# Optimization experiments

Hardware: AMD Instinct MI355X
Metric: run time of the kernel (lower is better)

The kernel has to match this reference:

```python
import jax, jax.numpy as jnp
import numpy as np

B, S, D = 2, 2048, 2048
H, KV, HD = 16, 8, 128
G = H // KV          # GQA group size
EPS = 1e-6
SCALE = HD ** -0.5


def setup_inputs() -> dict:
    key = jax.random.key(0)
    ks = jax.random.split(key, 8)
    x = jax.random.normal(ks[0], (B, S, D), dtype=jnp.float32)
    # RoPE tables (theta = 1e6, Qwen3-style), shape [B, S, HD]
    inv_freq = 1.0 / (1e6 ** (np.arange(0, HD, 2, dtype=np.float32) / HD))
    ang = np.arange(S, dtype=np.float32)[:, None] * inv_freq[None, :]   # [S, HD/2]
    emb = np.concatenate([ang, ang], axis=-1)                            # [S, HD]
    cos = jnp.broadcast_to(jnp.asarray(np.cos(emb)), (B, S, HD))
    sin = jnp.broadcast_to(jnp.asarray(np.sin(emb)), (B, S, HD))
    # additive causal mask [B, 1, S, S]
    causal = jnp.where(jnp.tril(jnp.ones((S, S), dtype=bool)), 0.0, -1e9).astype(jnp.float32)
    attention_mask = jnp.broadcast_to(causal[None, None], (B, 1, S, S))
    std = D ** -0.5
    wq = jax.random.normal(ks[1], (H * HD, D), dtype=jnp.float32) * std
    wk = jax.random.normal(ks[2], (KV * HD, D), dtype=jnp.float32) * std
    wv = jax.random.normal(ks[3], (KV * HD, D), dtype=jnp.float32) * std
    wo = jax.random.normal(ks[4], (D, H * HD), dtype=jnp.float32) * (H * HD) ** -0.5
    q_norm_w = jnp.ones((HD,), dtype=jnp.float32)
    k_norm_w = jnp.ones((HD,), dtype=jnp.float32)
    return {"x": x, "cos": cos, "sin": sin, "attention_mask": attention_mask,
            "wq": wq, "wk": wk, "wv": wv, "wo": wo,
            "q_norm_w": q_norm_w, "k_norm_w": k_norm_w}


def _rmsnorm(x, w):
    xf = x.astype(jnp.float32)
    var = jnp.mean(xf * xf, axis=-1, keepdims=True)
    return w * (xf * jax.lax.rsqrt(var + EPS)).astype(x.dtype)


def _rotate_half(x):
    x1, x2 = jnp.split(x, 2, axis=-1)
    return jnp.concatenate([-x2, x1], axis=-1)


def _rope(q, k, cos, sin):
    # q: [B,H,S,HD], k: [B,KV,S,HD]; cos/sin: [B,S,HD] -> [B,1,S,HD]
    c, s = cos[:, None], sin[:, None]
    return q * c + _rotate_half(q) * s, k * c + _rotate_half(k) * s


def reference(x, cos, sin, attention_mask, wq, wk, wv, wo, q_norm_w, k_norm_w):
    # projections -> [B, heads, S, HD]
    q = (x @ wq.T).reshape(B, S, H, HD).transpose(0, 2, 1, 3)
    k = (x @ wk.T).reshape(B, S, KV, HD).transpose(0, 2, 1, 3)
    v = (x @ wv.T).reshape(B, S, KV, HD).transpose(0, 2, 1, 3)
    q = _rmsnorm(q, q_norm_w)
    k = _rmsnorm(k, k_norm_w)
    q, k = _rope(q, k, cos, sin)
    # GQA: view q as [B, KV, G, S, HD]; contract against shared KV heads
    q5 = q.reshape(B, KV, G, S, HD)
    scores = jnp.einsum('bkgqd,bktd->bkgqt', q5, k) * SCALE       # [B,KV,G,S,S]
    scores = scores + attention_mask[:, :, None]                   # [B,1,1,S,S] broadcast
    attn = jax.nn.softmax(scores.astype(jnp.float32), axis=-1).astype(q.dtype)
    out = jnp.einsum('bkgqt,bktd->bkgqd', attn, v)                 # [B,KV,G,S,HD]
    out = out.reshape(B, H, S, HD).transpose(0, 2, 1, 3).reshape(B, S, H * HD)
    attn_output = out @ wo.T
    return attn_output, attn.reshape(B, H, S, S)
```

## Files before the change

kernel.cpp:

```cpp
#include <hip/hip_runtime.h>

#define B_  2
#define S_  2048
#define D_  2048
#define H_  16
#define KV_ 8
#define HD_ 128
#define SCALE_ 0.08838834764831845f

typedef __attribute__((ext_vector_type(8))) short sh8;
typedef __attribute__((ext_vector_type(4))) float f32x4;
typedef unsigned short u16;
typedef unsigned int u32;

__device__ __forceinline__ u16 f2bf(float f){
  u32 u = __float_as_uint(f);
  u += 0x7fffu + ((u >> 16) & 1u);
  return (u16)(u >> 16);
}
__device__ __forceinline__ float bf2f(u16 h){
  return __uint_as_float(((u32)h) << 16);
}
__device__ __forceinline__ void gl_lds16(const u16* g, u16* l){
  __builtin_amdgcn_global_load_lds(
      (const __attribute__((address_space(1))) u32*)g,
      (__attribute__((address_space(3))) u32*)l, 16, 0, 0);
}

__global__ void cvt_bf16(const float* __restrict__ in, u16* __restrict__ out, int n){
  int i = (blockIdx.x * blockDim.x + threadIdx.x) * 4;
  const int stride = gridDim.x * blockDim.x * 4;
  for (; i < n; i += stride){
    float4 f = *(const float4*)(in + i);
    ushort4 u;
    u.x = f2bf(f.x); u.y = f2bf(f.y); u.z = f2bf(f.z); u.w = f2bf(f.w);
    *(ushort4*)(out + i) = u;
  }
}

template<int MODE>
__global__ __launch_bounds__(256, 2) void gemm_bt(
    const u16* __restrict__ A, const u16* __restrict__ Bq,
    const u16* __restrict__ Bk, const u16* __restrict__ Bv,
    u16* __restrict__ Oq, u16* __restrict__ Ok, u16* __restrict__ Ov,
    float* __restrict__ Of, int K)
{
  __shared__ __align__(16) u16 As[128*32];
  __shared__ __align__(16) u16 Bs[128*32];
  const int m0 = blockIdx.y * 128, n0 = blockIdx.x * 128;
  const u16* Bp; int nb;
  if (MODE == 0){
    if      (n0 < 2048){ Bp = Bq; nb = n0;        }
    else if (n0 < 3072){ Bp = Bk; nb = n0 - 2048; }
    else               { Bp = Bv; nb = n0 - 3072; }
  } else { Bp = Bq; nb = n0; }
  const int tid = threadIdx.x, lane = tid & 63, w = tid >> 6;
  const int wr = w >> 1, wc = w & 1, lg = lane >> 4, l15 = lane & 15;
  const int srow = lane >> 2, skof = (lane & 3) * 8;
  f32x4 acc[4][4];
  #pragma unroll
  for (int i = 0; i < 4; ++i)
    #pragma unroll
    for (int j = 0; j < 4; ++j) acc[i][j] = (f32x4){0.f,0.f,0.f,0.f};
  const int nkt = K >> 5;
  for (int kt = 0; kt < nkt; ++kt){
    const int k0 = kt << 5;
    __syncthreads();
    #pragma unroll
    for (int c = 0; c < 2; ++c){
      const int chunk = w * 2 + c;
      gl_lds16(A  + (size_t)(m0 + chunk*16 + srow) * K + k0 + skof, As + chunk*512);
      gl_lds16(Bp + (size_t)(nb + chunk*16 + srow) * K + k0 + skof, Bs + chunk*512);
    }
    __syncthreads();
    sh8 af[4], bfr[4];
    #pragma unroll
    for (int mf = 0; mf < 4; ++mf) af[mf]  = *(const sh8*)(As + (wr*64 + mf*16 + l15)*32 + lg*8);
    #pragma unroll
    for (int nf = 0; nf < 4; ++nf) bfr[nf] = *(const sh8*)(Bs + (wc*64 + nf*16 + l15)*32 + lg*8);
    #pragma unroll
    for (int mf = 0; mf < 4; ++mf)
      #pragma unroll
      for (int nf = 0; nf < 4; ++nf)
        acc[mf][nf] = __builtin_amdgcn_mfma_f32_16x16x32_bf16(af[mf], bfr[nf], acc[mf][nf], 0, 0, 0);
  }
  #pragma unroll
  for (int mf = 0; mf < 4; ++mf)
    #pragma unroll
    for (int nf = 0; nf < 4; ++nf)
      #pragma unroll
      for (int r = 0; r < 4; ++r){
        const int row = m0 + wr*64 + mf*16 + lg*4 + r;
        const int col = n0 + wc*64 + nf*16 + l15;
        const float v = acc[mf][nf][r];
        if (MODE == 1){
          Of[(size_t)row * 2048 + col] = v;
        } else {
          const int b = row >> 11, s = row & 2047;
          const u16 u = f2bf(v);
          if (col < 2048){
            const int h = col >> 7, d = col & 127;
            Oq[((size_t)(b*H_ + h)*S_ + s)*HD_ + d] = u;
          } else if (col < 3072){
            const int kv = (col - 2048) >> 7, d = col & 127;
            Ok[((size_t)(b*KV_ + kv)*S_ + s)*HD_ + d] = u;
          } else {
            const int kv = (col - 3072) >> 7, d = col & 127;
            Ov[((size_t)(b*KV_ + kv)*S_ + s)*HD_ + d] = u;
          }
        }
      }
}

__global__ __launch_bounds__(256) void rmsrope(
    u16* __restrict__ qk, const float* __restrict__ cosb, const float* __restrict__ sinb,
    const float* __restrict__ wn, int nh)
{
  const int lane = threadIdx.x & 63;
  const int row  = blockIdx.x * 4 + (threadIdx.x >> 6);
  const int s    = row & (S_ - 1);
  const int b    = (row >> 11) / nh;
  u16* p = qk + (size_t)row * HD_;
  float x0 = bf2f(p[lane]), x1 = bf2f(p[lane + 64]);
  float ss = x0*x0 + x1*x1;
  #pragma unroll
  for (int mm = 1; mm < 64; mm <<= 1) ss += __shfl_xor(ss, mm, 64);
  const float rs = rsqrtf(ss * (1.0f/128.0f) + 1e-6f);
  const float n0 = x0 * rs * wn[lane], n1 = x1 * rs * wn[lane + 64];
  const float* cp = cosb + ((size_t)b*S_ + s)*HD_;
  const float* sp = sinb + ((size_t)b*S_ + s)*HD_;
  const float o0 = n0 * cp[lane]      - n1 * sp[lane];
  const float o1 = n1 * cp[lane + 64] + n0 * sp[lane + 64];
  p[lane] = f2bf(o0); p[lane + 64] = f2bf(o1);
}

__global__ __launch_bounds__(256, 2) void attn_stats(
    const u16* __restrict__ Q, const u16* __restrict__ Kc,
    float* __restrict__ mrow, float* __restrict__ lrow)
{
  __shared__ __align__(16) u16 Ks[64*136];
  const int qblk = blockIdx.x, bh = blockIdx.y;
  const int b = bh >> 4, h = bh & 15, kv = h >> 1;
  const u16* Qp = Q + ((size_t)(b*H_ + h)*S_ + qblk*64)*HD_;
  const u16* Kp = Kc + (size_t)(b*KV_ + kv)*S_*HD_;
  const int tid = threadIdx.x, lane = tid & 63, w = tid >> 6;
  const int lg = lane >> 4, l15 = lane & 15;
  sh8 aq[4];
  #pragma unroll
  for (int kk = 0; kk < 4; ++kk)
    aq[kk] = *(const sh8*)(Qp + (w*16 + l15)*HD_ + kk*32 + lg*8);
  float m_i[4] = {-1e30f,-1e30f,-1e30f,-1e30f};
  float l_i[4] = {0.f,0.f,0.f,0.f};
  const int row0 = qblk*64 + w*16 + lg*4;
  for (int jb = 0; jb <= qblk; ++jb){
    #pragma unroll
    for (int i = 0; i < 4; ++i){
      const int flat = tid + i*256;
      const int r = flat >> 4, kof = (flat & 15) * 8;
      *(sh8*)(Ks + r*136 + kof) = *(const sh8*)(Kp + (size_t)(jb*64 + r)*HD_ + kof);
    }
    __syncthreads();
    f32x4 sacc[4];
    #pragma unroll
    for (int nf = 0; nf < 4; ++nf) sacc[nf] = (f32x4){0.f,0.f,0.f,0.f};
    #pragma unroll
    for (int kk = 0; kk < 4; ++kk)
      #pragma unroll
      for (int nf = 0; nf < 4; ++nf){
        sh8 bk = *(const sh8*)(Ks + (nf*16 + l15)*136 + kk*32 + lg*8);
        sacc[nf] = __builtin_amdgcn_mfma_f32_16x16x32_bf16(aq[kk], bk, sacc[nf], 0, 0, 0);
      }
    __syncthreads();
    const bool diag = (jb == qblk);
    #pragma unroll
    for (int r = 0; r < 4; ++r){
      float sc[4]; float mx = -1e30f;
      #pragma unroll
      for (int nf = 0; nf < 4; ++nf){
        float v = sacc[nf][r] * SCALE_;
        if (diag && (jb*64 + nf*16 + l15) > (row0 + r)) v = -1e9f;
        sc[nf] = v; mx = fmaxf(mx, v);
      }
      #pragma unroll
      for (int mm = 1; mm < 16; mm <<= 1) mx = fmaxf(mx, __shfl_xor(mx, mm, 64));
      const float mnew = fmaxf(m_i[r], mx);
      float ps = __expf(sc[0]-mnew) + __expf(sc[1]-mnew) + __expf(sc[2]-mnew) + __expf(sc[3]-mnew);
      #pragma unroll
      for (int mm = 1; mm < 16; mm <<= 1) ps += __shfl_xor(ps, mm, 64);
      l_i[r] = l_i[r]*__expf(m_i[r]-mnew) + ps;
      m_i[r] = mnew;
    }
  }
  if (l15 == 0){
    #pragma unroll
    for (int r = 0; r < 4; ++r){
      const size_t gr = (size_t)(b*H_ + h)*S_ + row0 + r;
      mrow[gr] = m_i[r]; lrow[gr] = l_i[r];
    }
  }
}

__global__ __launch_bounds__(256, 2) void attn_pv(
    const u16* __restrict__ Q, const u16* __restrict__ Kc, const u16* __restrict__ V,
    const float* __restrict__ mrow, const float* __restrict__ lrow,
    float* __restrict__ attn, u16* __restrict__ Ob)
{
  __shared__ __align__(16) u16 Ks[64*136];
  __shared__ __align__(16) u16 Vt[128*72];
  __shared__ __align__(16) u16 Ps[64*72];
  const int qblk = blockIdx.x, bh = blockIdx.y;
  const int b = bh >> 4, h = bh & 15, kv = h >> 1;
  const u16* Qp = Q + ((size_t)(b*H_ + h)*S_ + qblk*64)*HD_;
  const u16* Kp = Kc + (size_t)(b*KV_ + kv)*S_*HD_;
  const u16* Vp = V  + (size_t)(b*KV_ + kv)*S_*HD_;
  const int tid = threadIdx.x, lane = tid & 63, w = tid >> 6;
  const int lg = lane >> 4, l15 = lane & 15;
  sh8 aq[4];
  #pragma unroll
  for (int kk = 0; kk < 4; ++kk)
    aq[kk] = *(const sh8*)(Qp + (w*16 + l15)*HD_ + kk*32 + lg*8);
  const int row0 = qblk*64 + w*16 + lg*4;
  float m4[4], linv[4];
  #pragma unroll
  for (int r = 0; r < 4; ++r){
    const size_t gr = (size_t)(b*H_ + h)*S_ + row0 + r;
    m4[r] = mrow[gr]; linv[r] = 1.0f / lrow[gr];
  }
  f32x4 o[8];
  #pragma unroll
  for (int i = 0; i < 8; ++i) o[i] = (f32x4){0.f,0.f,0.f,0.f};
  float* ab = attn + ((size_t)(b*H_ + h)*S_ + qblk*64)*S_;
  for (int jb = 0; jb <= qblk; ++jb){
    #pragma unroll
    for (int i = 0; i < 4; ++i){
      const int flat = tid + i*256;
      const int r = flat >> 4, kof = (flat & 15) * 8;
      *(sh8*)(Ks + r*136 + kof) = *(const sh8*)(Kp + (size_t)(jb*64 + r)*HD_ + kof);
      sh8 vv = *(const sh8*)(Vp + (size_t)(jb*64 + r)*HD_ + kof);
      #pragma unroll
      for (int e = 0; e < 8; ++e) Vt[(kof + e)*72 + r] = (u16)vv[e];
    }
    __syncthreads();
    f32x4 sacc[4];
    #pragma unroll
    for (int nf = 0; nf < 4; ++nf) sacc[nf] = (f32x4){0.f,0.f,0.f,0.f};
    #pragma unroll
    for (int kk = 0; kk < 4; ++kk)
      #pragma unroll
      for (int nf = 0; nf < 4; ++nf){
        sh8 bk = *(const sh8*)(Ks + (nf*16 + l15)*136 + kk*32 + lg*8);
        sacc[nf] = __builtin_amdgcn_mfma_f32_16x16x32_bf16(aq[kk], bk, sacc[nf], 0, 0, 0);
      }
    const bool diag = (jb == qblk);
    #pragma unroll
    for (int r = 0; r < 4; ++r)
      #pragma unroll
      for (int nf = 0; nf < 4; ++nf){
        const int col = jb*64 + nf*16 + l15;
        float v = sacc[nf][r] * SCALE_;
        if (diag && col > row0 + r) v = -1e9f;
        const float pn = __expf(v - m4[r]) * linv[r];
        ab[(size_t)(w*16 + lg*4 + r)*S_ + col] = pn;
        Ps[(w*16 + lg*4 + r)*72 + nf*16 + l15] = f2bf(pn);
      }
    #pragma unroll
    for (int kk = 0; kk < 2; ++kk){
      sh8 pa = *(const sh8*)(Ps + (w*16 + l15)*72 + kk*32 + lg*8);
      #pragma unroll
      for (int nf2 = 0; nf2 < 8; ++nf2){
        sh8 bv = *(const sh8*)(Vt + (nf2*16 + l15)*72 + kk*32 + lg*8);
        o[nf2] = __builtin_amdgcn_mfma_f32_16x16x32_bf16(pa, bv, o[nf2], 0, 0, 0);
      }
    }
    __syncthreads();
  }
  {
    const int c0 = (qblk + 1) * 64;
    const int nq = S_ - c0;
    if (nq > 0){
      const int quads = nq >> 2;
      const int total = 64 * quads;
      for (int idx = tid; idx < total; idx += 256){
        const int rr = idx / quads, cc = (idx % quads) * 4;
        *(float4*)(ab + (size_t)rr * S_ + c0 + cc) = make_float4(0.f,0.f,0.f,0.f);
      }
    }
  }
  #pragma unroll
  for (int nf2 = 0; nf2 < 8; ++nf2)
    #pragma unroll
    for (int r = 0; r < 4; ++r){
      const int sg = qblk*64 + w*16 + lg*4 + r;
      Ob[((size_t)(b*S_ + sg)*H_ + h)*HD_ + nf2*16 + l15] = f2bf(o[nf2][r]);
    }
}

extern "C" void kernel_launch(void* const* d_in, const int* in_sizes, int n_in,
                              void* d_out, int out_size, void* d_ws, size_t ws_size,
                              hipStream_t stream)
{
  const float* x    = (const float*)d_in[0];
  const float* cosp = (const float*)d_in[1];
  const float* sinp = (const float*)d_in[2];
  const float* wq   = (const float*)d_in[4];
  const float* wk   = (const float*)d_in[5];
  const float* wv   = (const float*)d_in[6];
  const float* wo   = (const float*)d_in[7];
  const float* qnw  = (const float*)d_in[8];
  const float* knw  = (const float*)d_in[9];

  const size_t N_X  = (size_t)B_*S_*D_;
  const size_t N_WQ = (size_t)H_*HD_*D_;
  const size_t N_WK = (size_t)KV_*HD_*D_;
  const size_t N_WO = (size_t)D_*H_*HD_;
  const size_t N_Q  = (size_t)B_*H_*S_*HD_;
  const size_t N_K  = (size_t)B_*KV_*S_*HD_;

  u16* xb  = (u16*)d_ws;
  u16* wqb = xb  + N_X;
  u16* wkb = wqb + N_WQ;
  u16* wvb = wkb + N_WK;
  u16* wob = wvb + N_WK;
  u16* qb  = wob + N_WO;
  u16* kb  = qb  + N_Q;
  u16* vb  = kb  + N_K;
  u16* ob  = vb  + N_K;
  float* mrow = (float*)(ob + N_X);
  float* lrow = mrow + (size_t)B_*H_*S_;

  float* out0 = (float*)d_out;
  float* attn = out0 + N_X;

  cvt_bf16<<<1024, 256, 0, stream>>>(x,  xb,  (int)N_X);
  cvt_bf16<<<512,  256, 0, stream>>>(wq, wqb, (int)N_WQ);
  cvt_bf16<<<256,  256, 0, stream>>>(wk, wkb, (int)N_WK);
  cvt_bf16<<<256,  256, 0, stream>>>(wv, wvb, (int)N_WK);
  cvt_bf16<<<512,  256, 0, stream>>>(wo, wob, (int)N_WO);

  gemm_bt<0><<<dim3(32, 32), 256, 0, stream>>>(xb, wqb, wkb, wvb, qb, kb, vb, nullptr, 2048);

  rmsrope<<<(B_*H_*S_)/4,  256, 0, stream>>>(qb, cosp, sinp, qnw, H_);
  rmsrope<<<(B_*KV_*S_)/4, 256, 0, stream>>>(kb, cosp, sinp, knw, KV_);

  attn_stats<<<dim3(S_/64, B_*H_), 256, 0, stream>>>(qb, kb, mrow, lrow);
  attn_pv  <<<dim3(S_/64, B_*H_), 256, 0, stream>>>(qb, kb, vb, mrow, lrow, attn, ob);

  gemm_bt<1><<<dim3(16, 32), 256, 0, stream>>>(ob, wob, nullptr, nullptr,
                                               nullptr, nullptr, nullptr, out0, 2048);
}
```

Baseline: 1.144 ms.

## Fuse attention stats and PV pass using unnormalized exp with deferred normalization

```diff
diff --git a/kernel.cpp b/kernel.cpp
--- a/kernel.cpp
+++ b/kernel.cpp
@@ -134,103 +134,36 @@
   p[lane] = f2bf(o0); p[lane + 64] = f2bf(o1);
 }
 
-__global__ __launch_bounds__(256, 2) void attn_stats(
-    const u16* __restrict__ Q, const u16* __restrict__ Kc,
-    float* __restrict__ mrow, float* __restrict__ lrow)
+__global__ __launch_bounds__(256, 2) void attn_fused(
+    const u16* __restrict__ Q, const u16* __restrict__ Kc, const u16* __restrict__ V,
+    u16* __restrict__ Pb, u16* __restrict__ Ob)
 {
   __shared__ __align__(16) u16 Ks[64*136];
-  const int qblk = blockIdx.x, bh = blockIdx.y;
+  __shared__ __align__(16) u16 Vt[128*72];
+  __shared__ __align__(16) u16 Ps[128*72];
+  const int qblk = (S_/128 - 1) - blockIdx.x;
+  const int bh = blockIdx.y;
   const int b = bh >> 4, h = bh & 15, kv = h >> 1;
-  const u16* Qp = Q + ((size_t)(b*H_ + h)*S_ + qblk*64)*HD_;
+  const u16* Qp = Q  + ((size_t)(b*H_ + h)*S_ + qblk*128)*HD_;
   const u16* Kp = Kc + (size_t)(b*KV_ + kv)*S_*HD_;
+  const u16* Vp = V  + (size_t)(b*KV_ + kv)*S_*HD_;
+  u16* Pq = Pb + ((size_t)(b*H_ + h)*S_ + qblk*128)*S_;
   const int tid = threadIdx.x, lane = tid & 63, w = tid >> 6;
   const int lg = lane >> 4, l15 = lane & 15;
-  sh8 aq[4];
-  #pragma unroll
-  for (int kk = 0; kk < 4; ++kk)
-    aq[kk] = *(const sh8*)(Qp + (w*16 + l15)*HD_ + kk*32 + lg*8);
-  float m_i[4] = {-1e30f,-1e30f,-1e30f,-1e30f};
-  float l_i[4] = {0.f,0.f,0.f,0.f};
-  const int row0 = qblk*64 + w*16 + lg*4;
-  for (int jb = 0; jb <= qblk; ++jb){
-    #pragma unroll
-    for (int i = 0; i < 4; ++i){
-      const int flat = tid + i*256;
-      const int r = flat >> 4, kof = (flat & 15) * 8;
-      *(sh8*)(Ks + r*136 + kof) = *(const sh8*)(Kp + (size_t)(jb*64 + r)*HD_ + kof);
-    }
-    __syncthreads();
-    f32x4 sacc[4];
-    #pragma unroll
-    for (int nf = 0; nf < 4; ++nf) sacc[nf] = (f32x4){0.f,0.f,0.f,0.f};
+  sh8 aq[2][4];
+  #pragma unroll
+  for (int mf = 0; mf < 2; ++mf)
     #pragma unroll
     for (int kk = 0; kk < 4; ++kk)
-      #pragma unroll
-      for (int nf = 0; nf < 4; ++nf){
-        sh8 bk = *(const sh8*)(Ks + (nf*16 + l15)*136 + kk*32 + lg*8);
-        sacc[nf] = __builtin_amdgcn_mfma_f32_16x16x32_bf16(aq[kk], bk, sacc[nf], 0, 0, 0);
-      }
-    __syncthreads();
-    const bool diag = (jb == qblk);
-    #pragma unroll
-    for (int r = 0; r < 4; ++r){
-      float sc[4]; float mx = -1e30f;
-      #pragma unroll
-      for (int nf = 0; nf < 4; ++nf){
-        float v = sacc[nf][r] * SCALE_;
-        if (diag && (jb*64 + nf*16 + l15) > (row0 + r)) v = -1e9f;
-        sc[nf] = v; mx = fmaxf(mx, v);
-      }
-      #pragma unroll
-      for (int mm = 1; mm < 16; mm <<= 1) mx = fmaxf(mx, __shfl_xor(mx, mm, 64));
-      const float mnew = fmaxf(m_i[r], mx);
-      float ps = __expf(sc[0]-mnew) + __expf(sc[1]-mnew) + __expf(sc[2]-mnew) + __expf(sc[3]-mnew);
-      #pragma unroll
-      for (int mm = 1; mm < 16; mm <<= 1) ps += __shfl_xor(ps, mm, 64);
-      l_i[r] = l_i[r]*__expf(m_i[r]-mnew) + ps;
-      m_i[r] = mnew;
-    }
-  }
-  if (l15 == 0){
-    #pragma unroll
-    for (int r = 0; r < 4; ++r){
-      const size_t gr = (size_t)(b*H_ + h)*S_ + row0 + r;
-      mrow[gr] = m_i[r]; lrow[gr] = l_i[r];
-    }
-  }
-}
-
-__global__ __launch_bounds__(256, 2) void attn_pv(
-    const u16* __restrict__ Q, const u16* __restrict__ Kc, const u16* __restrict__ V,
-    const float* __restrict__ mrow, const float* __restrict__ lrow,
-    float* __restrict__ attn, u16* __restrict__ Ob)
-{
-  __shared__ __align__(16) u16 Ks[64*136];
-  __shared__ __align__(16) u16 Vt[128*72];
-  __shared__ __align__(16) u16 Ps[64*72];
-  const int qblk = blockIdx.x, bh = blockIdx.y;
-  const int b = bh >> 4, h = bh & 15, kv = h >> 1;
-  const u16* Qp = Q + ((size_t)(b*H_ + h)*S_ + qblk*64)*HD_;
-  const u16* Kp = Kc + (size_t)(b*KV_ + kv)*S_*HD_;
-  const u16* Vp = V  + (size_t)(b*KV_ + kv)*S_*HD_;
-  const int tid = threadIdx.x, lane = tid & 63, w = tid >> 6;
-  const int lg = lane >> 4, l15 = lane & 15;
-  sh8 aq[4];
-  #pragma unroll
-  for (int kk = 0; kk < 4; ++kk)
-    aq[kk] = *(const sh8*)(Qp + (w*16 + l15)*HD_ + kk*32 + lg*8);
-  const int row0 = qblk*64 + w*16 + lg*4;
-  float m4[4], linv[4];
-  #pragma unroll
-  for (int r = 0; r < 4; ++r){
-    const size_t gr = (size_t)(b*H_ + h)*S_ + row0 + r;
-    m4[r] = mrow[gr]; linv[r] = 1.0f / lrow[gr];
-  }
-  f32x4 o[8];
-  #pragma unroll
-  for (int i = 0; i < 8; ++i) o[i] = (f32x4){0.f,0.f,0.f,0.f};
-  float* ab = attn + ((size_t)(b*H_ + h)*S_ + qblk*64)*S_;
-  for (int jb = 0; jb <= qblk; ++jb){
+      aq[mf][kk] = *(const sh8*)(Qp + (w*32 + mf*16 + l15)*HD_ + kk*32 + lg*8);
+  f32x4 o[2][8];
+  #pragma unroll
+  for (int mf = 0; mf < 2; ++mf)
+    #pragma unroll
+    for (int i = 0; i < 8; ++i) o[mf][i] = (f32x4){0.f,0.f,0.f,0.f};
+  const int jbmax = 2*qblk + 1;
+  for (int jb = 0; jb <= jbmax; ++jb){
+    __syncthreads();
     #pragma unroll
     for (int i = 0; i < 4; ++i){
       const int flat = tid + i*256;
@@ -241,58 +174,110 @@
       for (int e = 0; e < 8; ++e) Vt[(kof + e)*72 + r] = (u16)vv[e];
     }
     __syncthreads();
-    f32x4 sacc[4];
-    #pragma unroll
-    for (int nf = 0; nf < 4; ++nf) sacc[nf] = (f32x4){0.f,0.f,0.f,0.f};
+    f32x4 sacc[2][4];
+    #pragma unroll
+    for (int mf = 0; mf < 2; ++mf)
+      #pragma unroll
+      for (int nf = 0; nf < 4; ++nf) sacc[mf][nf] = (f32x4){0.f,0.f,0.f,0.f};
     #pragma unroll
     for (int kk = 0; kk < 4; ++kk)
       #pragma unroll
       for (int nf = 0; nf < 4; ++nf){
         sh8 bk = *(const sh8*)(Ks + (nf*16 + l15)*136 + kk*32 + lg*8);
-        sacc[nf] = __builtin_amdgcn_mfma_f32_16x16x32_bf16(aq[kk], bk, sacc[nf], 0, 0, 0);
+        #pragma unroll
+        for (int mf = 0; mf < 2; ++mf)
+          sacc[mf][nf] = __builtin_amdgcn_mfma_f32_16x16x32_bf16(aq[mf][kk], bk, sacc[mf][nf], 0, 0, 0);
       }
-    const bool diag = (jb == qblk);
-    #pragma unroll
-    for (int r = 0; r < 4; ++r)
-      #pragma unroll
-      for (int nf = 0; nf < 4; ++nf){
-        const int col = jb*64 + nf*16 + l15;
-        float v = sacc[nf][r] * SCALE_;
-        if (diag && col > row0 + r) v = -1e9f;
-        const float pn = __expf(v - m4[r]) * linv[r];
-        ab[(size_t)(w*16 + lg*4 + r)*S_ + col] = pn;
-        Ps[(w*16 + lg*4 + r)*72 + nf*16 + l15] = f2bf(pn);
+    const bool dblk = (jb >= 2*qblk);
+    #pragma unroll
+    for (int mf = 0; mf < 2; ++mf)
+      #pragma unroll
+      for (int nf = 0; nf < 4; ++nf)
+        #pragma unroll
+        for (int r = 0; r < 4; ++r){
+          const int row = qblk*128 + w*32 + mf*16 + lg*4 + r;
+          const int col = jb*64 + nf*16 + l15;
+          float p = __expf(sacc[mf][nf][r] * SCALE_);
+          if (dblk && col > row) p = 0.f;
+          Ps[(w*32 + mf*16 + lg*4 + r)*72 + nf*16 + l15] = f2bf(p);
+        }
+    #pragma unroll
+    for (int mf = 0; mf < 2; ++mf)
+      #pragma unroll
+      for (int kk = 0; kk < 2; ++kk){
+        sh8 pa = *(const sh8*)(Ps + (w*32 + mf*16 + l15)*72 + kk*32 + lg*8);
+        #pragma unroll
+        for (int nf2 = 0; nf2 < 8; ++nf2){
+          sh8 bv = *(const sh8*)(Vt + (nf2*16 + l15)*72 + kk*32 + lg*8);
+          o[mf][nf2] = __builtin_amdgcn_mfma_f32_16x16x32_bf16(pa, bv, o[mf][nf2], 0, 0, 0);
+        }
       }
-    #pragma unroll
-    for (int kk = 0; kk < 2; ++kk){
-      sh8 pa = *(const sh8*)(Ps + (w*16 + l15)*72 + kk*32 + lg*8);
-      #pragma unroll
-      for (int nf2 = 0; nf2 < 8; ++nf2){
-        sh8 bv = *(const sh8*)(Vt + (nf2*16 + l15)*72 + kk*32 + lg*8);
-        o[nf2] = __builtin_amdgcn_mfma_f32_16x16x32_bf16(pa, bv, o[nf2], 0, 0, 0);
+    __syncthreads();
+    #pragma unroll
+    for (int i = 0; i < 4; ++i){
+      const int id = tid + i*256;
+      const int row = id >> 3, cc = (id & 7) * 8;
+      *(sh8*)(Pq + (size_t)row*S_ + jb*64 + cc) = *(const sh8*)(Ps + row*72 + cc);
+    }
+  }
+  #pragma unroll
+  for (int mf = 0; mf < 2; ++mf)
+    #pragma unroll
+    for (int nf2 = 0; nf2 < 8; ++nf2)
+      #pragma unroll
+      for (int r = 0; r < 4; ++r){
+        const int sg = qblk*128 + w*32 + mf*16 + lg*4 + r;
+        Ob[((size_t)(b*S_ + sg)*H_ + h)*HD_ + nf2*16 + l15] = f2bf(o[mf][nf2][r]);
       }
+}
+
+__global__ __launch_bounds__(256) void prob_norm(
+    const u16* __restrict__ Pb, float* __restrict__ attn, float* __restrict__ invl)
+{
+  const int w = threadIdx.x >> 6, lane = threadIdx.x & 63;
+  const int row = blockIdx.x * 4 + w;
+  const int q = row & (S_ - 1);
+  const int nread = ((q >> 7) + 1) * 128;
+  const u16* pr = Pb + (size_t)row * S_;
+  float* ar = attn + (size_t)row * S_;
+  float pv[4][8];
+  float sum = 0.f;
+  #pragma unroll
+  for (int c = 0; c < 4; ++c){
+    const int col0 = c*512 + lane*8;
+    if (col0 < nread){
+      sh8 v = *(const sh8*)(pr + col0);
+      #pragma unroll
+      for (int e = 0; e < 8; ++e){ pv[c][e] = bf2f((u16)v[e]); sum += pv[c][e]; }
+    } else {
+      #pragma unroll
+      for (int e = 0; e < 8; ++e) pv[c][e] = 0.f;
     }
-    __syncthreads();
-  }
-  {
-    const int c0 = (qblk + 1) * 64;
-    const int nq = S_ - c0;
-    if (nq > 0){
-      const int quads = nq >> 2;
-      const int total = 64 * quads;
-      for (int idx = tid; idx < total; idx += 256){
-        const int rr = idx / quads, cc = (idx % quads) * 4;
-        *(float4*)(ab + (size_t)rr * S_ + c0 + cc) = make_float4(0.f,0.f,0.f,0.f);
-      }
-    }
-  }
-  #pragma unroll
-  for (int nf2 = 0; nf2 < 8; ++nf2)
-    #pragma unroll
-    for (int r = 0; r < 4; ++r){
-      const int sg = qblk*64 + w*16 + lg*4 + r;
-      Ob[((size_t)(b*S_ + sg)*H_ + h)*HD_ + nf2*16 + l15] = f2bf(o[nf2][r]);
-    }
+  }
+  #pragma unroll
+  for (int mm = 1; mm < 64; mm <<= 1) sum += __shfl_xor(sum, mm, 64);
+  const float inv = 1.0f / sum;
+  if (lane == 0) invl[row] = inv;
+  #pragma unroll
+  for (int c = 0; c < 4; ++c){
+    const int col0 = c*512 + lane*8;
+    float4 f0 = make_float4(pv[c][0]*inv, pv[c][1]*inv, pv[c][2]*inv, pv[c][3]*inv);
+    float4 f1 = make_float4(pv[c][4]*inv, pv[c][5]*inv, pv[c][6]*inv, pv[c][7]*inv);
+    *(float4*)(ar + col0)     = f0;
+    *(float4*)(ar + col0 + 4) = f1;
+  }
+}
+
+__global__ __launch_bounds__(256) void o_norm(u16* __restrict__ Ob, const float* __restrict__ invl){
+  const int idx = blockIdx.x * 256 + threadIdx.x;
+  const int rob = idx >> 4, d0 = (idx & 15) * 8;
+  const int h = rob & 15, s = (rob >> 4) & (S_-1), b = rob >> 15;
+  const float inv = invl[((size_t)(b*H_ + h))*S_ + s];
+  u16* p = Ob + (size_t)rob * HD_ + d0;
+  sh8 v = *(const sh8*)p;
+  #pragma unroll
+  for (int e = 0; e < 8; ++e) v[e] = (short)f2bf(bf2f((u16)v[e]) * inv);
+  *(sh8*)p = v;
 }
 
 extern "C" void kernel_launch(void* const* d_in, const int* in_sizes, int n_in,
@@ -315,6 +300,7 @@
   const size_t N_WO = (size_t)D_*H_*HD_;
   const size_t N_Q  = (size_t)B_*H_*S_*HD_;
   const size_t N_K  = (size_t)B_*KV_*S_*HD_;
+  const size_t N_P  = (size_t)B_*H_*S_*S_;
 
   u16* xb  = (u16*)d_ws;
   u16* wqb = xb  + N_X;
@@ -325,8 +311,8 @@
   u16* kb  = qb  + N_Q;
   u16* vb  = kb  + N_K;
   u16* ob  = vb  + N_K;
-  float* mrow = (float*)(ob + N_X);
-  float* lrow = mrow + (size_t)B_*H_*S_;
+  u16* Pb  = ob  + N_X;
+  float* invl = (float*)(Pb + N_P);
 
   float* out0 = (float*)d_out;
   float* attn = out0 + N_X;
@@ -342,8 +328,9 @@
   rmsrope<<<(B_*H_*S_)/4,  256, 0, stream>>>(qb, cosp, sinp, qnw, H_);
   rmsrope<<<(B_*KV_*S_)/4, 256, 0, stream>>>(kb, cosp, sinp, knw, KV_);
 
-  attn_stats<<<dim3(S_/64, B_*H_), 256, 0, stream>>>(qb, kb, mrow, lrow);
-  attn_pv  <<<dim3(S_/64, B_*H_), 256, 0, stream>>>(qb, kb, vb, mrow, lrow, attn, ob);
+  attn_fused<<<dim3(S_/128, B_*H_), 256, 0, stream>>>(qb, kb, vb, Pb, ob);
+  prob_norm <<<(B_*H_*S_)/4, 256, 0, stream>>>(Pb, attn, invl);
+  o_norm    <<<(B_*S_*H_*HD_/8)/256, 256, 0, stream>>>(ob, invl);
 
   gemm_bt<1><<<dim3(16, 32), 256, 0, stream>>>(ob, wob, nullptr, nullptr,
                                                nullptr, nullptr, nullptr, out0, 2048);
```

Result: faster. 1.059 ms (-7.4%).
